# Optimization experiments

Measured on AMD Instinct MI355X. Metric: run time of the kernel, lower is better.

Reference implementation:

```python
import jax, jax.numpy as jnp
import numpy as np

BATCH, D_MODEL, N_STATE, SEQ_L = 8, 1024, 64, 2048


def setup_inputs() -> dict:
    key = jax.random.key(0)
    k_u, k_a, k_b, k_c = jax.random.split(key, 4)
    scale = 1.0 / (D_MODEL * N_STATE) ** 0.5
    u = jax.random.normal(k_u, (BATCH, D_MODEL, SEQ_L), dtype=jnp.float32)
    # A is stored as a full NxN diagonal matrix, as in the torch module
    A = jnp.diag(jax.random.uniform(k_a, (N_STATE,), dtype=jnp.float32))
    B = jax.random.normal(k_b, (D_MODEL, N_STATE), dtype=jnp.float32) * scale
    C = jax.random.normal(k_c, (D_MODEL, N_STATE), dtype=jnp.float32) * scale
    return {"L": SEQ_L, "u": u, "A": A, "B": B, "C": C}


def reference(L, u, A, B, C):
    # u: (B, D, L). einsum('nn,bnd->bnd', A, h) in torch == diag(A) broadcast over h.
    a = jnp.diagonal(A)                       # (N,)
    Bu = jnp.einsum('dn,bdl->bnl', B, u)      # (B, N, L)
    Cu = jnp.einsum('dn,bdl->bnl', C, u)      # (B, N, L)
    bsz, d, _ = u.shape
    h0 = jnp.zeros((bsz, a.shape[0], d), dtype=u.dtype)  # (B, N, D)

    def step(h, xs):
        bu_l, cu_l, u_l = xs                  # (B,N), (B,N), (B,D)
        h = a[None, :, None] * h + bu_l[:, :, None] * u_l[:, None, :]
        y_l = jnp.einsum('bn,bnd->bd', cu_l, h)
        return h, y_l

    xs = (jnp.moveaxis(Bu, -1, 0), jnp.moveaxis(Cu, -1, 0), jnp.moveaxis(u, -1, 0))
    _, ys = jax.lax.scan(step, h0, xs)        # ys: (L, B, D)
    return jnp.moveaxis(ys, 0, -1)            # (B, D, L)
```

## Files before the change

### kernel.cpp

```cpp
#include <hip/hip_runtime.h>
#include <hip/hip_bf16.h>
#include <string.h>

#define BATCH 8
#define DM 1024
#define NS 64
#define SL 2048
#define NC 32
#define TC 64

typedef __attribute__((ext_vector_type(8))) short bf16x8;
typedef __attribute__((ext_vector_type(4))) float f32x4;
typedef float v2f __attribute__((ext_vector_type(2)));

__device__ inline unsigned short f2bf(float f) {
    union { float f; unsigned u; } v; v.f = f;
    return (unsigned short)((v.u + 0x7fffu + ((v.u >> 16) & 1u)) >> 16);
}
__device__ inline float bf2f(unsigned short h) {
    return __uint_as_float(((unsigned)h) << 16);
}
static __device__ inline v2f bfpair_to_v2f(unsigned int p) {
    unsigned int lo = p << 16, hi = p & 0xffff0000u;
    v2f r; r.x = __uint_as_float(lo); r.y = __uint_as_float(hi); return r;
}


__global__ __launch_bounds__(256) void k_prep(const float* __restrict__ Bm,
                                              const float* __restrict__ Cm,
                                              unsigned short* __restrict__ BT,
                                              unsigned short* __restrict__ CT)
{
    __shared__ float sT[64][65];
    const float* src = blockIdx.y ? Cm : Bm;
    unsigned short* dst = blockIdx.y ? CT : BT;
    const int d0 = blockIdx.x * 64, t = threadIdx.x;
    {
        int r = t >> 2, f = (t & 3) * 16;
#pragma unroll
        for (int i = 0; i < 4; i++) {
            float4 v = *(const float4*)&src[(size_t)(d0 + r) * NS + f + i * 4];
            sT[r][f + i * 4 + 0] = v.x; sT[r][f + i * 4 + 1] = v.y;
            sT[r][f + i * 4 + 2] = v.z; sT[r][f + i * 4 + 3] = v.w;
        }
    }
    __syncthreads();
    {
        int n = t >> 2, dq = (t & 3) * 16;
        unsigned pk[8];
#pragma unroll
        for (int k = 0; k < 8; k++) {
            unsigned short a = f2bf(sT[dq + 2 * k][n]);
            unsigned short bb = f2bf(sT[dq + 2 * k + 1][n]);
            pk[k] = (unsigned)a | ((unsigned)bb << 16);
        }
        uint4 v0 = { pk[0], pk[1], pk[2], pk[3] };
        uint4 v1 = { pk[4], pk[5], pk[6], pk[7] };
        *(uint4*)&dst[(size_t)n * DM + d0 + dq] = v0;
        *(uint4*)&dst[(size_t)n * DM + d0 + dq + 8] = v1;
    }
}

__global__ __launch_bounds__(512) void k_proj(const float* __restrict__ u,
                                              const unsigned short* __restrict__ BC,
                                              unsigned short* __restrict__ BuT,
                                              unsigned short* __restrict__ CuT,
                                              unsigned short* __restrict__ Ubf)
{
    __shared__ unsigned short sA[32 * 64];
    __shared__ unsigned short sB[128 * 64];
    const int b = blockIdx.y, l0 = blockIdx.x * 32, t = threadIdx.x;
    const int lane = t & 63, w = t >> 6, g = lane >> 4, m15 = lane & 15;
    const int dd = t >> 3, c8 = t & 7;
    const int dq = dd >> 3, d7 = dd & 7;

    f32x4 acc[2];
    acc[0] = (f32x4){0.f, 0.f, 0.f, 0.f};
    acc[1] = (f32x4){0.f, 0.f, 0.f, 0.f};

#pragma unroll 1
    for (int d0 = 0; d0 < DM; d0 += 64) {
        __syncthreads();
        {
            float4 v = *(const float4*)&u[((size_t)b * DM + d0 + dd) * SL + l0 + c8 * 4];
            unsigned short b0 = f2bf(v.x), b1 = f2bf(v.y), b2 = f2bf(v.z), b3 = f2bf(v.w);
            int l = c8 * 4;
            sA[(l + 0) * 64 + ((dq ^ ((l + 0) & 7)) * 8) + d7] = b0;
            sA[(l + 1) * 64 + ((dq ^ ((l + 1) & 7)) * 8) + d7] = b1;
            sA[(l + 2) * 64 + ((dq ^ ((l + 2) & 7)) * 8) + d7] = b2;
            sA[(l + 3) * 64 + ((dq ^ ((l + 3) & 7)) * 8) + d7] = b3;
            uint2 pk = { (unsigned)b0 | ((unsigned)b1 << 16),
                         (unsigned)b2 | ((unsigned)b3 << 16) };
            *(uint2*)(Ubf + ((size_t)b * DM + d0 + dd) * SL + l0 + c8 * 4) = pk;
        }
#pragma unroll
        for (int p = 0; p < 2; p++) {
            int idx = p * 512 + t;
            int row = idx >> 3, cc8 = idx & 7;
            uint4 v = *(const uint4*)(BC + (size_t)row * DM + d0 + cc8 * 8);
            *(uint4*)&sB[row * 64 + ((cc8 ^ (row & 7)) * 8)] = v;
        }
        __syncthreads();
#pragma unroll
        for (int ks = 0; ks < 2; ks++) {
            bf16x8 af[2], bfr;
#pragma unroll
            for (int mt = 0; mt < 2; mt++) {
                int r = mt * 16 + m15;
                af[mt] = *(const bf16x8*)&sA[r * 64 + (((ks * 4 + g) ^ (r & 7)) * 8)];
            }
            {
                int r = w * 16 + m15;
                bfr = *(const bf16x8*)&sB[r * 64 + (((ks * 4 + g) ^ (r & 7)) * 8)];
            }
#pragma unroll
            for (int mt = 0; mt < 2; mt++)
                acc[mt] = __builtin_amdgcn_mfma_f32_16x16x32_bf16(af[mt], bfr, acc[mt], 0, 0, 0);
        }
    }
    {
        int wn = w * 16 + m15;
        unsigned short* dst = (wn < 64) ? BuT : CuT;
        int n = wn & 63;
#pragma unroll
        for (int mt = 0; mt < 2; mt++)
#pragma unroll
            for (int r = 0; r < 4; r++) {
                int l = l0 + mt * 16 + g * 4 + r;
                dst[((size_t)b * SL + l) * NS + n] = f2bf(acc[mt][r]);
            }
    }
}

__global__ __launch_bounds__(256) void k_g(const float* __restrict__ A,
                                           const unsigned short* __restrict__ BuT,
                                           const unsigned short* __restrict__ CuT,
                                           unsigned short* __restrict__ Gw,
                                           unsigned short* __restrict__ Bvw,
                                           unsigned short* __restrict__ Wcw)
{
    __shared__ unsigned short sCu[64 * 64];
    __shared__ unsigned short sBu[8 * 64 * 8];
    __shared__ unsigned short sP[8 * 66 * 8];
    __shared__ unsigned short sTb[64 * 66];
    const int cc = blockIdx.x, b = cc >> 5, c = cc & 31;
    const int gy = blockIdx.y;
    const int t = threadIdx.x, lane = t & 63;
    const int l0 = c * TC;
    const size_t gbase = (size_t)cc * 4096;

    {
        const unsigned short* srcC = CuT + ((size_t)b * SL + l0) * NS;
        const unsigned short* srcB = BuT + ((size_t)b * SL + l0) * NS;
#pragma unroll
        for (int p = 0; p < 2; p++) {
            int idx = p * 256 + t;
            int r = idx >> 3, q8 = idx & 7;
            uint4 vc = *(const uint4*)(srcC + (size_t)r * NS + q8 * 8);
            *(uint4*)&sCu[r * 64 + q8 * 8] = vc;
            uint4 vb = *(const uint4*)(srcB + (size_t)r * NS + q8 * 8);
            *(uint4*)&sBu[(q8 * 64 + r) * 8] = vb;
        }
    }
    {
        int n = t & 63;
        float an = A[n * NS + n];
        int q = n >> 3, n7 = n & 7;
#pragma unroll 1
        for (int dl = (t >> 6) * 17; dl < (t >> 6) * 17 + 17 && dl <= 64; dl++)
            sP[(q * 66 + dl) * 8 + n7] = f2bf(__powf(an, (float)dl));
    }
    __syncthreads();

#pragma unroll 1
    for (int r = gy * 8; r < gy * 8 + 8; r++) {
        int idx = r * 256 + t;
        int l = idx >> 6;
        int lp = lane;
        int dl = l - lp;
        float acc = 0.f;
        if (dl >= 0) {
#pragma unroll
            for (int q = 0; q < 8; q++) {
                bf16x8 cu = *(const bf16x8*)&sCu[l * 64 + q * 8];
                bf16x8 bu = *(const bf16x8*)&sBu[(q * 64 + lp) * 8];
                bf16x8 pp = *(const bf16x8*)&sP[(q * 66 + dl) * 8];
#pragma unroll
                for (int j = 0; j < 8; j++)
                    acc = fmaf(bf2f((unsigned short)cu[j]) * bf2f((unsigned short)bu[j]),
                               bf2f((unsigned short)pp[j]), acc);
            }
        }
        Gw[gbase + l * 64 + lp] = (dl >= 0) ? f2bf(acc) : (unsigned short)0;
    }

    if (gy == 0) {
#pragma unroll 1
        for (int r = 0; r < 16; r++) {
            int idx = r * 256 + t;
            int l = idx >> 6;
            int n = lane, q = n >> 3, n7 = n & 7;
            float cu = bf2f(sCu[l * 64 + n]);
            float pv = bf2f(sP[(q * 66 + (l + 1)) * 8 + n7]);
            Wcw[gbase + l * 64 + n] = f2bf(cu * pv);
        }
    } else {
#pragma unroll 1
        for (int r = 0; r < 16; r++) {
            int idx = r * 256 + t;
            int l = idx >> 6;
            int n = lane, q = n >> 3, n7 = n & 7;
            float bu = bf2f(sBu[(q * 64 + l) * 8 + n7]);
            float pv = bf2f(sP[(q * 66 + (63 - l)) * 8 + n7]);
            sTb[n * 66 + l] = f2bf(bu * pv);
        }
        __syncthreads();
#pragma unroll 1
        for (int r = 0; r < 16; r++) {
            int idx = r * 256 + t;
            int n = idx >> 6;
            int l = lane;
            Bvw[gbase + n * 64 + l] = sTb[n * 66 + l];
        }
    }
}

__global__ __launch_bounds__(256) void k_state(const unsigned short* __restrict__ Ubf,
                                               const unsigned short* __restrict__ Bvw,
                                               unsigned short* __restrict__ Ew)
{
    __shared__ unsigned short sU[256 * 64];
    __shared__ unsigned short sV[64 * 64];
    const int slab = blockIdx.x, c = blockIdx.y, b = blockIdx.z;
    const int d0 = slab * 256, l0 = c * TC;
    const int t = threadIdx.x, lane = t & 63, w = t >> 6, g = lane >> 4, m15 = lane & 15;

    {
        size_t gbase = ((size_t)(b * NC + c)) * 4096;
        int rr = t >> 3, c8 = t & 7;
#pragma unroll
        for (int p = 0; p < 2; p++) {
            int r = p * 32 + rr;
            uint4 vv = *(const uint4*)(Bvw + gbase + r * 64 + c8 * 8);
            *(uint4*)&sV[r * 64 + ((c8 ^ (r & 7)) * 8)] = vv;
        }
    }
    {
        const unsigned short* usrc = Ubf + ((size_t)b * DM + d0) * SL + l0;
#pragma unroll
        for (int p = 0; p < 8; p++) {
            int idx = p * 256 + t;
            int dd = idx >> 3, q8 = idx & 7;
            uint4 v = *(const uint4*)(usrc + (size_t)dd * SL + q8 * 8);
            *(uint4*)&sU[dd * 64 + ((q8 ^ (dd & 7)) * 8)] = v;
        }
    }
    __syncthreads();

    f32x4 accE[4][4];
#pragma unroll
    for (int i = 0; i < 4; i++)
#pragma unroll
        for (int j = 0; j < 4; j++) accE[i][j] = (f32x4){0.f, 0.f, 0.f, 0.f};

#pragma unroll
    for (int ks = 0; ks < 2; ks++) {
        bf16x8 af[4];
#pragma unroll
        for (int mt = 0; mt < 4; mt++) {
            int r = w * 64 + mt * 16 + m15;
            af[mt] = *(const bf16x8*)&sU[r * 64 + (((ks * 4 + g) ^ (r & 7)) * 8)];
        }
#pragma unroll
        for (int nt = 0; nt < 4; nt++) {
            int rg = nt * 16 + m15;
            bf16x8 bv = *(const bf16x8*)&sV[rg * 64 + (((ks * 4 + g) ^ (rg & 7)) * 8)];
#pragma unroll
            for (int mt = 0; mt < 4; mt++)
                accE[mt][nt] = __builtin_amdgcn_mfma_f32_16x16x32_bf16(af[mt], bv, accE[mt][nt], 0, 0, 0);
        }
    }
#pragma unroll
    for (int mt = 0; mt < 4; mt++)
#pragma unroll
        for (int nt = 0; nt < 4; nt++)
#pragma unroll
            for (int r = 0; r < 4; r++) {
                int d = d0 + w * 64 + mt * 16 + g * 4 + r;
                Ew[(((size_t)b * NC + c) * DM + d) * NS + nt * 16 + m15] = f2bf(accE[mt][nt][r]);
            }
}

__global__ __launch_bounds__(256) void k_prefix(const float* __restrict__ A,
                                                unsigned short* __restrict__ E)
{
    int gg = blockIdx.x * 256 + threadIdx.x;
    int p  = gg & 31;
    int d  = (gg >> 5) & (DM - 1);
    int b  = gg >> 15;
    int n0 = p * 2;

    float a0 = A[n0 * NS + n0];
    float a1 = A[(n0 + 1) * NS + (n0 + 1)];
    v2f aT = { __powf(a0, (float)TC), __powf(a1, (float)TC) };
    v2f hs = { 0.f, 0.f };

    unsigned int* base = (unsigned int*)E + ((((size_t)b * NC) * DM + d) * NS >> 1) + p;
    const size_t cstride = ((size_t)DM * NS) >> 1;

#pragma unroll 4
    for (int c = 0; c < NC; c++) {
        unsigned int* ptr = base + (size_t)c * cstride;
        unsigned int e = *ptr;
        unsigned int sw = (unsigned)f2bf(hs.x) | ((unsigned)f2bf(hs.y) << 16);
        *ptr = sw;
        hs = __builtin_elementwise_fma(aT, hs, bfpair_to_v2f(e));
    }
}

__global__ __launch_bounds__(256) void k_y(const unsigned short* __restrict__ Ubf,
                                           const unsigned short* __restrict__ Gw,
                                           const unsigned short* __restrict__ Wcw,
                                           const unsigned short* __restrict__ HS,
                                           float* __restrict__ y)
{
    __shared__ unsigned short sU[256 * 64];
    __shared__ unsigned short sG[64 * 64];
    __shared__ unsigned short sW[64 * 64];
    const int slab = blockIdx.x, c = blockIdx.y, b = blockIdx.z;
    const int d0 = slab * 256, l0 = c * TC;
    const int t = threadIdx.x, lane = t & 63, w = t >> 6, g = lane >> 4, m15 = lane & 15;

    {
        size_t gbase = ((size_t)(b * NC + c)) * 4096;
        int rr = t >> 3, c8 = t & 7;
#pragma unroll
        for (int p = 0; p < 2; p++) {
            int r = p * 32 + rr;
            uint4 gv = *(const uint4*)(Gw + gbase + r * 64 + c8 * 8);
            *(uint4*)&sG[r * 64 + ((c8 ^ (r & 7)) * 8)] = gv;
            uint4 wv = *(const uint4*)(Wcw + gbase + r * 64 + c8 * 8);
            *(uint4*)&sW[r * 64 + ((c8 ^ (r & 7)) * 8)] = wv;
        }
    }
    {
        const unsigned short* usrc = Ubf + ((size_t)b * DM + d0) * SL + l0;
#pragma unroll
        for (int p = 0; p < 8; p++) {
            int idx = p * 256 + t;
            int dd = idx >> 3, q8 = idx & 7;
            uint4 v = *(const uint4*)(usrc + (size_t)dd * SL + q8 * 8);
            *(uint4*)&sU[dd * 64 + ((q8 ^ (dd & 7)) * 8)] = v;
        }
    }
    __syncthreads();

    f32x4 acc[4][4];
#pragma unroll
    for (int i = 0; i < 4; i++)
#pragma unroll
        for (int j = 0; j < 4; j++) acc[i][j] = (f32x4){0.f, 0.f, 0.f, 0.f};

    const unsigned short* hbase = HS + (((size_t)b * NC + c) * DM + d0) * NS;

#pragma unroll
    for (int ks = 0; ks < 2; ks++) {
        bf16x8 af[4];
#pragma unroll
        for (int mt = 0; mt < 4; mt++) {
            int r = w * 64 + mt * 16 + m15;
            af[mt] = *(const bf16x8*)&sU[r * 64 + (((ks * 4 + g) ^ (r & 7)) * 8)];
        }
#pragma unroll
        for (int nt = 0; nt < 4; nt++) {
            int rg = nt * 16 + m15;
            bf16x8 bg = *(const bf16x8*)&sG[rg * 64 + (((ks * 4 + g) ^ (rg & 7)) * 8)];
#pragma unroll
            for (int mt = 0; mt < 4; mt++)
                acc[mt][nt] = __builtin_amdgcn_mfma_f32_16x16x32_bf16(af[mt], bg, acc[mt][nt], 0, 0, 0);
        }
    }
#pragma unroll
    for (int ks = 0; ks < 2; ks++) {
        bf16x8 ah[4];
#pragma unroll
        for (int mt = 0; mt < 4; mt++) {
            int r = w * 64 + mt * 16 + m15;
            ah[mt] = *(const bf16x8*)(hbase + (size_t)r * NS + (ks * 4 + g) * 8);
        }
#pragma unroll
        for (int nt = 0; nt < 4; nt++) {
            int rg = nt * 16 + m15;
            bf16x8 bw = *(const bf16x8*)&sW[rg * 64 + (((ks * 4 + g) ^ (rg & 7)) * 8)];
#pragma unroll
            for (int mt = 0; mt < 4; mt++)
                acc[mt][nt] = __builtin_amdgcn_mfma_f32_16x16x32_bf16(ah[mt], bw, acc[mt][nt], 0, 0, 0);
        }
    }
#pragma unroll
    for (int mt = 0; mt < 4; mt++)
#pragma unroll
        for (int nt = 0; nt < 4; nt++)
#pragma unroll
            for (int r = 0; r < 4; r++) {
                int d = d0 + w * 64 + mt * 16 + g * 4 + r;
                int l = l0 + nt * 16 + m15;
                y[((size_t)b * DM + d) * SL + l] = acc[mt][nt][r];
            }
}

extern "C" void kernel_launch(void* const* d_in, const int* in_sizes, int n_in,
                              void* d_out, int out_size, void* d_ws, size_t ws_size,
                              hipStream_t stream) {
    const float* u = (const float*)d_in[1];
    const float* A = (const float*)d_in[2];
    const float* B = (const float*)d_in[3];
    const float* C = (const float*)d_in[4];
    float* y = (float*)d_out;

    char* base = (char*)d_ws;
    unsigned short* BuT = (unsigned short*)(base);
    unsigned short* CuT = (unsigned short*)(base + (2u << 20));
    unsigned short* BT  = (unsigned short*)(base + (4u << 20));
    unsigned short* Gw  = (unsigned short*)(base + (5u << 20));
    unsigned short* Bvw = (unsigned short*)(base + (7u << 20));
    unsigned short* Wcw = (unsigned short*)(base + (9u << 20));
    unsigned short* Ew  = (unsigned short*)(base + (11u << 20));
    unsigned short* Ubf = (unsigned short*)(base + (44u << 20));
    unsigned short* CT  = BT + (size_t)NS * DM;

    k_prep<<<dim3(DM / 64, 2), 256, 0, stream>>>(B, C, BT, CT);
    k_proj<<<dim3(SL / 32, BATCH), 512, 0, stream>>>(u, BT, BuT, CuT, Ubf);
    k_g<<<dim3(BATCH * NC, 2), 256, 0, stream>>>(A, BuT, CuT, Gw, Bvw, Wcw);
    k_state<<<dim3(4, NC, BATCH), 256, 0, stream>>>(Ubf, Bvw, Ew);
    k_prefix<<<dim3(BATCH * DM * 32 / 256), 256, 0, stream>>>(A, Ew);
    k_y<<<dim3(4, NC, BATCH), 256, 0, stream>>>(Ubf, Gw, Wcw, Ew, y);
}
```

Measured before the change: 104.0 us.

## Fuse chunk state, prefix scan and output into one sequential-chunk kernel

Replaces the three kernels k_state, k_prefix and k_y with a single kernel. Each block owns 32 channels of one batch, walks the 32 chunks in order, keeps the running state in registers and shared memory, and prefetches the next chunk's operands while the current chunk computes. This removes the global round trip of the bf16 chunk-state tensor and two kernel launches. In exchange the grid drops to 256 blocks with a serial 32-step loop and two block-wide barriers per step, which reduces parallelism and latency hiding.

```diff
diff --git a/kernel.cpp b/kernel.cpp
--- a/kernel.cpp
+++ b/kernel.cpp
@@ -11,7 +11,6 @@
 
 typedef __attribute__((ext_vector_type(8))) short bf16x8;
 typedef __attribute__((ext_vector_type(4))) float f32x4;
-typedef float v2f __attribute__((ext_vector_type(2)));
 
 __device__ inline unsigned short f2bf(float f) {
     union { float f; unsigned u; } v; v.f = f;
@@ -19,10 +18,6 @@
 }
 __device__ inline float bf2f(unsigned short h) {
     return __uint_as_float(((unsigned)h) << 16);
-}
-static __device__ inline v2f bfpair_to_v2f(unsigned int p) {
-    unsigned int lo = p << 16, hi = p & 0xffff0000u;
-    v2f r; r.x = __uint_as_float(lo); r.y = __uint_as_float(hi); return r;
 }
 
 
@@ -225,188 +220,120 @@
     }
 }
 
-__global__ __launch_bounds__(256) void k_state(const unsigned short* __restrict__ Ubf,
+__global__ __launch_bounds__(256) void k_scan2(const unsigned short* __restrict__ Ubf,
+                                               const unsigned short* __restrict__ Gw,
                                                const unsigned short* __restrict__ Bvw,
-                                               unsigned short* __restrict__ Ew)
+                                               const unsigned short* __restrict__ Wcw,
+                                               const float* __restrict__ A,
+                                               float* __restrict__ y)
 {
-    __shared__ unsigned short sU[256 * 64];
+    __shared__ unsigned short sU[32 * 64];
+    __shared__ unsigned short sG[64 * 64];
     __shared__ unsigned short sV[64 * 64];
-    const int slab = blockIdx.x, c = blockIdx.y, b = blockIdx.z;
-    const int d0 = slab * 256, l0 = c * TC;
+    __shared__ unsigned short sW[64 * 64];
+    __shared__ unsigned short sH[32 * 64];
+    const int slab = blockIdx.x, b = blockIdx.y;
+    const int d0 = slab * 32;
     const int t = threadIdx.x, lane = t & 63, w = t >> 6, g = lane >> 4, m15 = lane & 15;
-
-    {
-        size_t gbase = ((size_t)(b * NC + c)) * 4096;
-        int rr = t >> 3, c8 = t & 7;
+    const int rr = t >> 3, c8 = t & 7;
+
+    const int n_own = w * 16 + m15;
+    const float pw = __powf(A[n_own * NS + n_own], (float)TC);
+
+    *(uint4*)&sH[t * 8] = (uint4){0u, 0u, 0u, 0u};
+    float hsf[8];
+#pragma unroll
+    for (int i = 0; i < 8; i++) hsf[i] = 0.f;
+
+    const unsigned short* ub = Ubf + ((size_t)b * DM + d0 + rr) * SL + c8 * 8;
+    const size_t gb0 = ((size_t)b * NC) * 4096;
+
+    uint4 pU, pG[2], pV[2], pW[2];
+    pU = *(const uint4*)(ub);
+#pragma unroll
+    for (int p = 0; p < 2; p++) {
+        size_t ro = (size_t)(p * 32 + rr) * 64 + c8 * 8;
+        pG[p] = *(const uint4*)(Gw + gb0 + ro);
+        pV[p] = *(const uint4*)(Bvw + gb0 + ro);
+        pW[p] = *(const uint4*)(Wcw + gb0 + ro);
+    }
+
+#pragma unroll 1
+    for (int c = 0; c < NC; c++) {
+        *(uint4*)&sU[rr * 64 + ((c8 ^ (rr & 7)) * 8)] = pU;
 #pragma unroll
         for (int p = 0; p < 2; p++) {
-            int r = p * 32 + rr;
-            uint4 vv = *(const uint4*)(Bvw + gbase + r * 64 + c8 * 8);
-            *(uint4*)&sV[r * 64 + ((c8 ^ (r & 7)) * 8)] = vv;
-        }
-    }
-    {
-        const unsigned short* usrc = Ubf + ((size_t)b * DM + d0) * SL + l0;
-#pragma unroll
-        for (int p = 0; p < 8; p++) {
-            int idx = p * 256 + t;
-            int dd = idx >> 3, q8 = idx & 7;
-            uint4 v = *(const uint4*)(usrc + (size_t)dd * SL + q8 * 8);
-            *(uint4*)&sU[dd * 64 + ((q8 ^ (dd & 7)) * 8)] = v;
-        }
-    }
-    __syncthreads();
-
-    f32x4 accE[4][4];
-#pragma unroll
-    for (int i = 0; i < 4; i++)
-#pragma unroll
-        for (int j = 0; j < 4; j++) accE[i][j] = (f32x4){0.f, 0.f, 0.f, 0.f};
-
-#pragma unroll
-    for (int ks = 0; ks < 2; ks++) {
-        bf16x8 af[4];
-#pragma unroll
-        for (int mt = 0; mt < 4; mt++) {
-            int r = w * 64 + mt * 16 + m15;
-            af[mt] = *(const bf16x8*)&sU[r * 64 + (((ks * 4 + g) ^ (r & 7)) * 8)];
-        }
-#pragma unroll
-        for (int nt = 0; nt < 4; nt++) {
-            int rg = nt * 16 + m15;
-            bf16x8 bv = *(const bf16x8*)&sV[rg * 64 + (((ks * 4 + g) ^ (rg & 7)) * 8)];
-#pragma unroll
-            for (int mt = 0; mt < 4; mt++)
-                accE[mt][nt] = __builtin_amdgcn_mfma_f32_16x16x32_bf16(af[mt], bv, accE[mt][nt], 0, 0, 0);
-        }
-    }
-#pragma unroll
-    for (int mt = 0; mt < 4; mt++)
-#pragma unroll
-        for (int nt = 0; nt < 4; nt++)
-#pragma unroll
-            for (int r = 0; r < 4; r++) {
-                int d = d0 + w * 64 + mt * 16 + g * 4 + r;
-                Ew[(((size_t)b * NC + c) * DM + d) * NS + nt * 16 + m15] = f2bf(accE[mt][nt][r]);
-            }
-}
-
-__global__ __launch_bounds__(256) void k_prefix(const float* __restrict__ A,
-                                                unsigned short* __restrict__ E)
-{
-    int gg = blockIdx.x * 256 + threadIdx.x;
-    int p  = gg & 31;
-    int d  = (gg >> 5) & (DM - 1);
-    int b  = gg >> 15;
-    int n0 = p * 2;
-
-    float a0 = A[n0 * NS + n0];
-    float a1 = A[(n0 + 1) * NS + (n0 + 1)];
-    v2f aT = { __powf(a0, (float)TC), __powf(a1, (float)TC) };
-    v2f hs = { 0.f, 0.f };
-
-    unsigned int* base = (unsigned int*)E + ((((size_t)b * NC) * DM + d) * NS >> 1) + p;
-    const size_t cstride = ((size_t)DM * NS) >> 1;
-
-#pragma unroll 4
-    for (int c = 0; c < NC; c++) {
-        unsigned int* ptr = base + (size_t)c * cstride;
-        unsigned int e = *ptr;
-        unsigned int sw = (unsigned)f2bf(hs.x) | ((unsigned)f2bf(hs.y) << 16);
-        *ptr = sw;
-        hs = __builtin_elementwise_fma(aT, hs, bfpair_to_v2f(e));
-    }
-}
-
-__global__ __launch_bounds__(256) void k_y(const unsigned short* __restrict__ Ubf,
-                                           const unsigned short* __restrict__ Gw,
-                                           const unsigned short* __restrict__ Wcw,
-                                           const unsigned short* __restrict__ HS,
-                                           float* __restrict__ y)
-{
-    __shared__ unsigned short sU[256 * 64];
-    __shared__ unsigned short sG[64 * 64];
-    __shared__ unsigned short sW[64 * 64];
-    const int slab = blockIdx.x, c = blockIdx.y, b = blockIdx.z;
-    const int d0 = slab * 256, l0 = c * TC;
-    const int t = threadIdx.x, lane = t & 63, w = t >> 6, g = lane >> 4, m15 = lane & 15;
-
-    {
-        size_t gbase = ((size_t)(b * NC + c)) * 4096;
-        int rr = t >> 3, c8 = t & 7;
-#pragma unroll
-        for (int p = 0; p < 2; p++) {
-            int r = p * 32 + rr;
-            uint4 gv = *(const uint4*)(Gw + gbase + r * 64 + c8 * 8);
-            *(uint4*)&sG[r * 64 + ((c8 ^ (r & 7)) * 8)] = gv;
-            uint4 wv = *(const uint4*)(Wcw + gbase + r * 64 + c8 * 8);
-            *(uint4*)&sW[r * 64 + ((c8 ^ (r & 7)) * 8)] = wv;
-        }
-    }
-    {
-        const unsigned short* usrc = Ubf + ((size_t)b * DM + d0) * SL + l0;
-#pragma unroll
-        for (int p = 0; p < 8; p++) {
-            int idx = p * 256 + t;
-            int dd = idx >> 3, q8 = idx & 7;
-            uint4 v = *(const uint4*)(usrc + (size_t)dd * SL + q8 * 8);
-            *(uint4*)&sU[dd * 64 + ((q8 ^ (dd & 7)) * 8)] = v;
-        }
-    }
-    __syncthreads();
-
-    f32x4 acc[4][4];
-#pragma unroll
-    for (int i = 0; i < 4; i++)
-#pragma unroll
-        for (int j = 0; j < 4; j++) acc[i][j] = (f32x4){0.f, 0.f, 0.f, 0.f};
-
-    const unsigned short* hbase = HS + (((size_t)b * NC + c) * DM + d0) * NS;
-
-#pragma unroll
-    for (int ks = 0; ks < 2; ks++) {
-        bf16x8 af[4];
-#pragma unroll
-        for (int mt = 0; mt < 4; mt++) {
-            int r = w * 64 + mt * 16 + m15;
-            af[mt] = *(const bf16x8*)&sU[r * 64 + (((ks * 4 + g) ^ (r & 7)) * 8)];
-        }
-#pragma unroll
-        for (int nt = 0; nt < 4; nt++) {
-            int rg = nt * 16 + m15;
-            bf16x8 bg = *(const bf16x8*)&sG[rg * 64 + (((ks * 4 + g) ^ (rg & 7)) * 8)];
-#pragma unroll
-            for (int mt = 0; mt < 4; mt++)
-                acc[mt][nt] = __builtin_amdgcn_mfma_f32_16x16x32_bf16(af[mt], bg, acc[mt][nt], 0, 0, 0);
-        }
-    }
-#pragma unroll
-    for (int ks = 0; ks < 2; ks++) {
-        bf16x8 ah[4];
-#pragma unroll
-        for (int mt = 0; mt < 4; mt++) {
-            int r = w * 64 + mt * 16 + m15;
-            ah[mt] = *(const bf16x8*)(hbase + (size_t)r * NS + (ks * 4 + g) * 8);
-        }
-#pragma unroll
-        for (int nt = 0; nt < 4; nt++) {
-            int rg = nt * 16 + m15;
-            bf16x8 bw = *(const bf16x8*)&sW[rg * 64 + (((ks * 4 + g) ^ (rg & 7)) * 8)];
-#pragma unroll
-            for (int mt = 0; mt < 4; mt++)
-                acc[mt][nt] = __builtin_amdgcn_mfma_f32_16x16x32_bf16(ah[mt], bw, acc[mt][nt], 0, 0, 0);
-        }
-    }
-#pragma unroll
-    for (int mt = 0; mt < 4; mt++)
-#pragma unroll
-        for (int nt = 0; nt < 4; nt++)
-#pragma unroll
-            for (int r = 0; r < 4; r++) {
-                int d = d0 + w * 64 + mt * 16 + g * 4 + r;
-                int l = l0 + nt * 16 + m15;
-                y[((size_t)b * DM + d) * SL + l] = acc[mt][nt][r];
-            }
+            int row = p * 32 + rr;
+            *(uint4*)&sG[row * 64 + ((c8 ^ (row & 7)) * 8)] = pG[p];
+            *(uint4*)&sV[row * 64 + ((c8 ^ (row & 7)) * 8)] = pV[p];
+            *(uint4*)&sW[row * 64 + ((c8 ^ (row & 7)) * 8)] = pW[p];
+        }
+        __syncthreads();
+
+        if (c + 1 < NC) {
+            pU = *(const uint4*)(ub + (c + 1) * 64);
+            size_t gb = gb0 + (size_t)(c + 1) * 4096;
+#pragma unroll
+            for (int p = 0; p < 2; p++) {
+                size_t ro = (size_t)(p * 32 + rr) * 64 + c8 * 8;
+                pG[p] = *(const uint4*)(Gw + gb + ro);
+                pV[p] = *(const uint4*)(Bvw + gb + ro);
+                pW[p] = *(const uint4*)(Wcw + gb + ro);
+            }
+        }
+
+        f32x4 accY[2], accE[2];
+        accY[0] = (f32x4){0.f, 0.f, 0.f, 0.f}; accY[1] = accY[0];
+        accE[0] = accY[0]; accE[1] = accY[0];
+
+#pragma unroll
+        for (int ks = 0; ks < 2; ks++) {
+            int kq = ks * 4 + g;
+            int r0 = m15, r1 = 16 + m15;
+            int rg = w * 16 + m15;
+            bf16x8 af0 = *(const bf16x8*)&sU[r0 * 64 + ((kq ^ (r0 & 7)) * 8)];
+            bf16x8 af1 = *(const bf16x8*)&sU[r1 * 64 + ((kq ^ (r1 & 7)) * 8)];
+            bf16x8 ah0 = *(const bf16x8*)&sH[r0 * 64 + ((kq ^ (r0 & 7)) * 8)];
+            bf16x8 ah1 = *(const bf16x8*)&sH[r1 * 64 + ((kq ^ (r1 & 7)) * 8)];
+            bf16x8 bg  = *(const bf16x8*)&sG[rg * 64 + ((kq ^ (rg & 7)) * 8)];
+            bf16x8 bw_ = *(const bf16x8*)&sW[rg * 64 + ((kq ^ (rg & 7)) * 8)];
+            bf16x8 bv  = *(const bf16x8*)&sV[rg * 64 + ((kq ^ (rg & 7)) * 8)];
+            accY[0] = __builtin_amdgcn_mfma_f32_16x16x32_bf16(af0, bg,  accY[0], 0, 0, 0);
+            accY[1] = __builtin_amdgcn_mfma_f32_16x16x32_bf16(af1, bg,  accY[1], 0, 0, 0);
+            accY[0] = __builtin_amdgcn_mfma_f32_16x16x32_bf16(ah0, bw_, accY[0], 0, 0, 0);
+            accY[1] = __builtin_amdgcn_mfma_f32_16x16x32_bf16(ah1, bw_, accY[1], 0, 0, 0);
+            accE[0] = __builtin_amdgcn_mfma_f32_16x16x32_bf16(af0, bv,  accE[0], 0, 0, 0);
+            accE[1] = __builtin_amdgcn_mfma_f32_16x16x32_bf16(af1, bv,  accE[1], 0, 0, 0);
+        }
+
+        {
+            float* yb = y + ((size_t)b * DM + d0 + g * 4) * SL + c * 64 + w * 16 + m15;
+#pragma unroll
+            for (int mt = 0; mt < 2; mt++)
+#pragma unroll
+                for (int r = 0; r < 4; r++)
+                    yb[(size_t)(mt * 16 + r) * SL] = accY[mt][r];
+        }
+
+#pragma unroll
+        for (int mt = 0; mt < 2; mt++)
+#pragma unroll
+            for (int r = 0; r < 4; r++)
+                hsf[mt * 4 + r] = fmaf(pw, hsf[mt * 4 + r], accE[mt][r]);
+
+        __syncthreads();
+
+        if (c + 1 < NC) {
+            int nq = n_own >> 3, n7 = n_own & 7;
+#pragma unroll
+            for (int mt = 0; mt < 2; mt++)
+#pragma unroll
+                for (int r = 0; r < 4; r++) {
+                    int dd = mt * 16 + g * 4 + r;
+                    sH[dd * 64 + ((nq ^ (dd & 7)) * 8) + n7] = f2bf(hsf[mt * 4 + r]);
+                }
+        }
+    }
 }
 
 extern "C" void kernel_launch(void* const* d_in, const int* in_sizes, int n_in,
@@ -425,14 +352,11 @@
     unsigned short* Gw  = (unsigned short*)(base + (5u << 20));
     unsigned short* Bvw = (unsigned short*)(base + (7u << 20));
     unsigned short* Wcw = (unsigned short*)(base + (9u << 20));
-    unsigned short* Ew  = (unsigned short*)(base + (11u << 20));
     unsigned short* Ubf = (unsigned short*)(base + (44u << 20));
     unsigned short* CT  = BT + (size_t)NS * DM;
 
     k_prep<<<dim3(DM / 64, 2), 256, 0, stream>>>(B, C, BT, CT);
     k_proj<<<dim3(SL / 32, BATCH), 512, 0, stream>>>(u, BT, BuT, CuT, Ubf);
     k_g<<<dim3(BATCH * NC, 2), 256, 0, stream>>>(A, BuT, CuT, Gw, Bvw, Wcw);
-    k_state<<<dim3(4, NC, BATCH), 256, 0, stream>>>(Ubf, Bvw, Ew);
-    k_prefix<<<dim3(BATCH * DM * 32 / 256), 256, 0, stream>>>(A, Ew);
-    k_y<<<dim3(4, NC, BATCH), 256, 0, stream>>>(Ubf, Gw, Wcw, Ew, y);
-}
+    k_scan2<<<dim3(DM / 32, BATCH), 256, 0, stream>>>(Ubf, Gw, Bvw, Wcw, A, y);
+}
```

Result: slower. 119.0 us (+14.4%).

## Halve d-slab per block and load U fragments directly from global

Applied to the files above, without the earlier changes.

In k_state and k_y, each block now covers 128 d-rows instead of 256, doubling the grid to 8×NC×BATCH. The 32 KB shared U tile and its staging copy are removed, and MFMA A-fragments are read straight from global memory, since each U row chunk is used by one wave only. This aims to cut LDS footprint and staging overhead and to raise occupancy and parallelism. In exchange, the G/W/V tiles are reloaded twice as often, and the uncoalesced-looking strided global reads may cost bandwidth.

```diff
diff --git a/kernel.cpp b/kernel.cpp
--- a/kernel.cpp
+++ b/kernel.cpp
@@ -229,10 +229,9 @@
                                                const unsigned short* __restrict__ Bvw,
                                                unsigned short* __restrict__ Ew)
 {
-    __shared__ unsigned short sU[256 * 64];
     __shared__ unsigned short sV[64 * 64];
     const int slab = blockIdx.x, c = blockIdx.y, b = blockIdx.z;
-    const int d0 = slab * 256, l0 = c * TC;
+    const int d0 = slab * 128, l0 = c * TC;
     const int t = threadIdx.x, lane = t & 63, w = t >> 6, g = lane >> 4, m15 = lane & 15;
 
     {
@@ -245,48 +244,41 @@
             *(uint4*)&sV[r * 64 + ((c8 ^ (r & 7)) * 8)] = vv;
         }
     }
-    {
-        const unsigned short* usrc = Ubf + ((size_t)b * DM + d0) * SL + l0;
-#pragma unroll
-        for (int p = 0; p < 8; p++) {
-            int idx = p * 256 + t;
-            int dd = idx >> 3, q8 = idx & 7;
-            uint4 v = *(const uint4*)(usrc + (size_t)dd * SL + q8 * 8);
-            *(uint4*)&sU[dd * 64 + ((q8 ^ (dd & 7)) * 8)] = v;
-        }
-    }
     __syncthreads();
 
-    f32x4 accE[4][4];
-#pragma unroll
-    for (int i = 0; i < 4; i++)
+    const unsigned short* ub = Ubf + ((size_t)b * DM + d0) * SL + l0;
+
+    f32x4 accE[2][4];
+#pragma unroll
+    for (int i = 0; i < 2; i++)
 #pragma unroll
         for (int j = 0; j < 4; j++) accE[i][j] = (f32x4){0.f, 0.f, 0.f, 0.f};
 
 #pragma unroll
     for (int ks = 0; ks < 2; ks++) {
-        bf16x8 af[4];
-#pragma unroll
-        for (int mt = 0; mt < 4; mt++) {
-            int r = w * 64 + mt * 16 + m15;
-            af[mt] = *(const bf16x8*)&sU[r * 64 + (((ks * 4 + g) ^ (r & 7)) * 8)];
+        int kq = ks * 4 + g;
+        bf16x8 af[2];
+#pragma unroll
+        for (int mt = 0; mt < 2; mt++) {
+            int r = w * 32 + mt * 16 + m15;
+            af[mt] = *(const bf16x8*)(ub + (size_t)r * SL + kq * 8);
         }
 #pragma unroll
         for (int nt = 0; nt < 4; nt++) {
             int rg = nt * 16 + m15;
-            bf16x8 bv = *(const bf16x8*)&sV[rg * 64 + (((ks * 4 + g) ^ (rg & 7)) * 8)];
-#pragma unroll
-            for (int mt = 0; mt < 4; mt++)
+            bf16x8 bv = *(const bf16x8*)&sV[rg * 64 + ((kq ^ (rg & 7)) * 8)];
+#pragma unroll
+            for (int mt = 0; mt < 2; mt++)
                 accE[mt][nt] = __builtin_amdgcn_mfma_f32_16x16x32_bf16(af[mt], bv, accE[mt][nt], 0, 0, 0);
         }
     }
 #pragma unroll
-    for (int mt = 0; mt < 4; mt++)
+    for (int mt = 0; mt < 2; mt++)
 #pragma unroll
         for (int nt = 0; nt < 4; nt++)
 #pragma unroll
             for (int r = 0; r < 4; r++) {
-                int d = d0 + w * 64 + mt * 16 + g * 4 + r;
+                int d = d0 + w * 32 + mt * 16 + g * 4 + r;
                 Ew[(((size_t)b * NC + c) * DM + d) * NS + nt * 16 + m15] = f2bf(accE[mt][nt][r]);
             }
 }
@@ -324,11 +316,10 @@
                                            const unsigned short* __restrict__ HS,
                                            float* __restrict__ y)
 {
-    __shared__ unsigned short sU[256 * 64];
     __shared__ unsigned short sG[64 * 64];
     __shared__ unsigned short sW[64 * 64];
     const int slab = blockIdx.x, c = blockIdx.y, b = blockIdx.z;
-    const int d0 = slab * 256, l0 = c * TC;
+    const int d0 = slab * 128, l0 = c * TC;
     const int t = threadIdx.x, lane = t & 63, w = t >> 6, g = lane >> 4, m15 = lane & 15;
 
     {
@@ -343,67 +334,60 @@
             *(uint4*)&sW[r * 64 + ((c8 ^ (r & 7)) * 8)] = wv;
         }
     }
-    {
-        const unsigned short* usrc = Ubf + ((size_t)b * DM + d0) * SL + l0;
-#pragma unroll
-        for (int p = 0; p < 8; p++) {
-            int idx = p * 256 + t;
-            int dd = idx >> 3, q8 = idx & 7;
-            uint4 v = *(const uint4*)(usrc + (size_t)dd * SL + q8 * 8);
-            *(uint4*)&sU[dd * 64 + ((q8 ^ (dd & 7)) * 8)] = v;
-        }
-    }
     __syncthreads();
 
-    f32x4 acc[4][4];
-#pragma unroll
-    for (int i = 0; i < 4; i++)
+    const unsigned short* ub    = Ubf + ((size_t)b * DM + d0) * SL + l0;
+    const unsigned short* hbase = HS + (((size_t)b * NC + c) * DM + d0) * NS;
+
+    f32x4 acc[2][4];
+#pragma unroll
+    for (int i = 0; i < 2; i++)
 #pragma unroll
         for (int j = 0; j < 4; j++) acc[i][j] = (f32x4){0.f, 0.f, 0.f, 0.f};
 
-    const unsigned short* hbase = HS + (((size_t)b * NC + c) * DM + d0) * NS;
-
 #pragma unroll
     for (int ks = 0; ks < 2; ks++) {
-        bf16x8 af[4];
-#pragma unroll
-        for (int mt = 0; mt < 4; mt++) {
-            int r = w * 64 + mt * 16 + m15;
-            af[mt] = *(const bf16x8*)&sU[r * 64 + (((ks * 4 + g) ^ (r & 7)) * 8)];
+        int kq = ks * 4 + g;
+        bf16x8 af[2];
+#pragma unroll
+        for (int mt = 0; mt < 2; mt++) {
+            int r = w * 32 + mt * 16 + m15;
+            af[mt] = *(const bf16x8*)(ub + (size_t)r * SL + kq * 8);
         }
 #pragma unroll
         for (int nt = 0; nt < 4; nt++) {
             int rg = nt * 16 + m15;
-            bf16x8 bg = *(const bf16x8*)&sG[rg * 64 + (((ks * 4 + g) ^ (rg & 7)) * 8)];
-#pragma unroll
-            for (int mt = 0; mt < 4; mt++)
+            bf16x8 bg = *(const bf16x8*)&sG[rg * 64 + ((kq ^ (rg & 7)) * 8)];
+#pragma unroll
+            for (int mt = 0; mt < 2; mt++)
                 acc[mt][nt] = __builtin_amdgcn_mfma_f32_16x16x32_bf16(af[mt], bg, acc[mt][nt], 0, 0, 0);
         }
     }
 #pragma unroll
     for (int ks = 0; ks < 2; ks++) {
-        bf16x8 ah[4];
-#pragma unroll
-        for (int mt = 0; mt < 4; mt++) {
-            int r = w * 64 + mt * 16 + m15;
-            ah[mt] = *(const bf16x8*)(hbase + (size_t)r * NS + (ks * 4 + g) * 8);
+        int kq = ks * 4 + g;
+        bf16x8 ah[2];
+#pragma unroll
+        for (int mt = 0; mt < 2; mt++) {
+            int r = w * 32 + mt * 16 + m15;
+            ah[mt] = *(const bf16x8*)(hbase + (size_t)r * NS + kq * 8);
         }
 #pragma unroll
         for (int nt = 0; nt < 4; nt++) {
             int rg = nt * 16 + m15;
-            bf16x8 bw = *(const bf16x8*)&sW[rg * 64 + (((ks * 4 + g) ^ (rg & 7)) * 8)];
-#pragma unroll
-            for (int mt = 0; mt < 4; mt++)
+            bf16x8 bw = *(const bf16x8*)&sW[rg * 64 + ((kq ^ (rg & 7)) * 8)];
+#pragma unroll
+            for (int mt = 0; mt < 2; mt++)
                 acc[mt][nt] = __builtin_amdgcn_mfma_f32_16x16x32_bf16(ah[mt], bw, acc[mt][nt], 0, 0, 0);
         }
     }
 #pragma unroll
-    for (int mt = 0; mt < 4; mt++)
+    for (int mt = 0; mt < 2; mt++)
 #pragma unroll
         for (int nt = 0; nt < 4; nt++)
 #pragma unroll
             for (int r = 0; r < 4; r++) {
-                int d = d0 + w * 64 + mt * 16 + g * 4 + r;
+                int d = d0 + w * 32 + mt * 16 + g * 4 + r;
                 int l = l0 + nt * 16 + m15;
                 y[((size_t)b * DM + d) * SL + l] = acc[mt][nt][r];
             }
@@ -432,7 +416,7 @@
     k_prep<<<dim3(DM / 64, 2), 256, 0, stream>>>(B, C, BT, CT);
     k_proj<<<dim3(SL / 32, BATCH), 512, 0, stream>>>(u, BT, BuT, CuT, Ubf);
     k_g<<<dim3(BATCH * NC, 2), 256, 0, stream>>>(A, BuT, CuT, Gw, Bvw, Wcw);
-    k_state<<<dim3(4, NC, BATCH), 256, 0, stream>>>(Ubf, Bvw, Ew);
+    k_state<<<dim3(8, NC, BATCH), 256, 0, stream>>>(Ubf, Bvw, Ew);
     k_prefix<<<dim3(BATCH * DM * 32 / 256), 256, 0, stream>>>(A, Ew);
-    k_y<<<dim3(4, NC, BATCH), 256, 0, stream>>>(Ubf, Gw, Wcw, Ew, y);
-}
+    k_y<<<dim3(8, NC, BATCH), 256, 0, stream>>>(Ubf, Gw, Wcw, Ew, y);
+}
```

After: 108.1 us. 1.04x slower.
